# Optimization experiments

Hardware: AMD Instinct MI355X
Metric: run time of the kernel (lower is better)

Reference implementation:

```python
import jax, jax.numpy as jnp
import numpy as np

B, S = 2, 2048
D, H, L = 768, 12, 2
DH = D // H
WIN = 128            # one-sided sliding window
C = WIN              # query chunk size
NC = S // C
FF = 4 * D
V = 50265
SEP_ID = 2
NSEP = 16
G = NSEP + 1         # CLS + all SEP tokens are global
NCLS = 7
HID = 100
NEG = -1e9
SEP_POS = np.arange(1, NSEP + 1) * 120   # fixed [SEP] layout, same every row


def setup_inputs() -> dict:
    key = jax.random.key(0)
    ks = iter(jax.random.split(key, 32))
    def p(shape, scale=0.02):
        return scale * jax.random.normal(next(ks), shape, jnp.float32)
    input_ids = jax.random.randint(next(ks), (B, S), 10, V)
    input_ids = input_ids.at[:, SEP_POS].set(SEP_ID)
    attention_mask = jnp.ones((B, S), jnp.int32)
    return dict(
        input_ids=input_ids, attention_mask=attention_mask,
        tok_emb=p((V, D)), pos_emb=p((S, D)),
        ln_e_g=jnp.ones((D,)), ln_e_b=jnp.zeros((D,)),
        Wq=p((L, D, D)), bq=jnp.zeros((L, D)),
        Wk=p((L, D, D)), bk=jnp.zeros((L, D)),
        Wv=p((L, D, D)), bv=jnp.zeros((L, D)),
        Wo=p((L, D, D)), bo=jnp.zeros((L, D)),
        ln1_g=jnp.ones((L, D)), ln1_b=jnp.zeros((L, D)),
        W1=p((L, D, FF)), b1=jnp.zeros((L, FF)),
        W2=p((L, FF, D)), b2=jnp.zeros((L, D)),
        ln2_g=jnp.ones((L, D)), ln2_b=jnp.zeros((L, D)),
        Wh=p((2 * D, HID)), bh=jnp.zeros((HID,)),
        Wout=p((HID, NCLS)), bout=jnp.zeros((NCLS,)),
    )


def _ln(x, g, b):
    mu = jnp.mean(x, -1, keepdims=True)
    var = jnp.var(x, -1, keepdims=True)
    return (x - mu) * jax.lax.rsqrt(var + 1e-5) * g + b


def forward(input_ids, attention_mask, tok_emb, pos_emb, ln_e_g, ln_e_b,
            Wq, bq, Wk, bk, Wv, bv, Wo, bo, ln1_g, ln1_b,
            W1, b1, W2, b2, ln2_g, ln2_b, Wh, bh, Wout, bout):
    # global positions: CLS + every [SEP] (same layout in every row)
    sep_pos = jnp.nonzero(input_ids[0] == SEP_ID, size=NSEP)[0]          # [NSEP]
    glob = jnp.concatenate([jnp.zeros((1,), sep_pos.dtype), sep_pos])    # [G]

    amask = attention_mask.astype(jnp.float32)                           # [B,S]
    is_glob = jnp.zeros((S,), bool).at[glob].set(True)

    # banded (sliding-window) gather pattern, padded-coordinate indices
    idx = jnp.arange(NC)[:, None] * C + jnp.arange(3 * C)[None, :]       # [NC,3C]
    pos_k = idx - C                                                      # abs key pos
    pos_q = jnp.arange(NC)[:, None] * C + jnp.arange(C)[None, :]         # [NC,C]
    pos_k_c = jnp.clip(pos_k, 0, S - 1)
    band = jnp.abs(pos_k[:, None, :] - pos_q[:, :, None]) <= WIN         # [NC,C,3C]
    inb = (pos_k >= 0) & (pos_k < S)                                     # [NC,3C]
    # global keys are handled by the dedicated global columns -> drop from band
    band = band & (inb & ~is_glob[pos_k_c])[:, None, :]
    km = amask[:, pos_k_c] * inb                                         # [B,NC,3C]
    valid = band[None] & (km[:, :, None, :] > 0)                         # [B,NC,C,3C]
    gmask = amask[:, glob] > 0                                           # [B,G]

    x = tok_emb[input_ids] + pos_emb[None]                               # [B,S,D]
    x = _ln(x, ln_e_g, ln_e_b)

    for l in range(L):
        q = (x @ Wq[l] + bq[l]).reshape(B, S, H, DH).transpose(0, 2, 1, 3) * (DH ** -0.5)
        k = (x @ Wk[l] + bk[l]).reshape(B, S, H, DH).transpose(0, 2, 1, 3)
        v = (x @ Wv[l] + bv[l]).reshape(B, S, H, DH).transpose(0, 2, 1, 3)
        kp = jnp.pad(k, ((0, 0), (0, 0), (C, C), (0, 0)))
        vp = jnp.pad(v, ((0, 0), (0, 0), (C, C), (0, 0)))
        k3 = kp[:, :, idx]                                               # [B,H,NC,3C,DH]
        v3 = vp[:, :, idx]
        qc = q.reshape(B, H, NC, C, DH)
        s_loc = jnp.einsum('bhncd,bhnkd->bhnck', qc, k3)                 # banded scores
        s_loc = jnp.where(valid[:, None], s_loc, NEG)
        kg, vg = k[:, :, glob], v[:, :, glob]                            # [B,H,G,DH]
        s_g = jnp.einsum('bhncd,bhgd->bhncg', qc, kg)
        s_g = jnp.where(gmask[:, None, None, None, :], s_g, NEG)
        p = jax.nn.softmax(jnp.concatenate([s_loc, s_g], axis=-1), axis=-1)
        out = (jnp.einsum('bhnck,bhnkd->bhncd', p[..., :3 * C], v3)
               + jnp.einsum('bhncg,bhgd->bhncd', p[..., 3 * C:], vg))
        out = out.reshape(B, H, S, DH)
        # global query rows attend to the full sequence
        qg = q[:, :, glob]
        s_full = jnp.einsum('bhgd,bhsd->bhgs', qg, k)
        s_full = jnp.where(amask[:, None, None, :] > 0, s_full, NEG)
        out_g = jnp.einsum('bhgs,bhsd->bhgd', jax.nn.softmax(s_full, -1), v)
        out = out.at[:, :, glob, :].set(out_g)
        a = out.transpose(0, 2, 1, 3).reshape(B, S, D) @ Wo[l] + bo[l]
        x = _ln(x + a, ln1_g[l], ln1_b[l])
        h = jax.nn.gelu(x @ W1[l] + b1[l])
        x = _ln(x + h @ W2[l] + b2[l], ln2_g[l], ln2_b[l])

    # core-sentence embeddings: hstack(CLS, interior SEP embeddings)
    core = sep_pos[1:-1]                                                 # [NSEP-2]
    cls = x[:, 0, :]                                                     # [B,D]
    seps = x[:, core, :]                                                 # [B,NSEP-2,D]
    emb = jnp.concatenate([jnp.broadcast_to(cls[:, None], seps.shape), seps], -1)
    emb = emb.reshape(B * (NSEP - 2), 2 * D)
    return jax.nn.relu(emb @ Wh + bh) @ Wout + bout                      # [28, NCLS]


def reference(input_ids, attention_mask, tok_emb, pos_emb, ln_e_g, ln_e_b,
              Wq, bq, Wk, bk, Wv, bv, Wo, bo, ln1_g, ln1_b,
              W1, b1, W2, b2, ln2_g, ln2_b, Wh, bh, Wout, bout):
    return forward(input_ids, attention_mask, tok_emb, pos_emb, ln_e_g, ln_e_b,
                   Wq, bq, Wk, bk, Wv, bv, Wo, bo, ln1_g, ln1_b,
                   W1, b1, W2, b2, ln2_g, ln2_b, Wh, bh, Wout, bout)
```

## Files before the change

kernel.cpp:

```cpp
#include <hip/hip_runtime.h>
#include <hip/hip_bf16.h>
#include <math.h>

#define Sdim 2048
#define Bdim 2
#define Ddim 768
#define Hdim 12
#define DHdim 64
#define Ldim 2
#define Cdim 128
#define NCdim 16
#define FFdim 3072
#define Gdim 17
#define NSEPd 16
#define HIDd 100
#define NCLSd 7
#define SEPID 2
#define MROWS (Bdim*Sdim)
#define QKVS 2304
#define MNSZ (MROWS*Ddim)

typedef __bf16 bf16_t;
typedef bf16_t bf16x8 __attribute__((ext_vector_type(8)));
typedef float f32x4 __attribute__((ext_vector_type(4)));
typedef ushort ushort8v __attribute__((ext_vector_type(8)));

__device__ __forceinline__ ushort f2bf(float f) {
    union { float f; unsigned u; } a; a.f = f;
    unsigned u = a.u;
    unsigned r = (u + 0x7fffu + ((u >> 16) & 1u)) >> 16;
    return (ushort)r;
}
__device__ __forceinline__ float bf2f(ushort h) {
    union { unsigned u; float f; } a; a.u = ((unsigned)h) << 16;
    return a.f;
}
__device__ __forceinline__ void gload16(const ushort* g, ushort* l) {
    __builtin_amdgcn_global_load_lds(
        (const __attribute__((address_space(1))) void*)g,
        (__attribute__((address_space(3))) void*)l, 16, 0, 0);
}

__global__ __launch_bounds__(1024) void k_findsep(const int* __restrict__ ids,
        int* __restrict__ glob, int* __restrict__ isg,
        const float* __restrict__ bq, const float* __restrict__ bk,
        const float* __restrict__ bv, float* __restrict__ bqkv) {
    __shared__ unsigned long long mw[32];
    __shared__ int pfx[32];
    int t = threadIdx.x;
    int flg[2];
    #pragma unroll
    for (int pass = 0; pass < 2; ++pass) {
        int p = pass * 1024 + t;
        int f = (ids[p] == SEPID);
        flg[pass] = f;
        unsigned long long m = __ballot(f);
        if ((t & 63) == 0) mw[pass * 16 + (t >> 6)] = m;
    }
    __syncthreads();
    if (t == 0) {
        int c = 0;
        #pragma unroll
        for (int i = 0; i < 32; ++i) { pfx[i] = c; c += __popcll(mw[i]); }
        glob[0] = 0;
    }
    __syncthreads();
    #pragma unroll
    for (int pass = 0; pass < 2; ++pass) {
        int p = pass * 1024 + t;
        int w = pass * 16 + (t >> 6);
        int lane = t & 63;
        int rank = pfx[w] + __popcll(mw[w] & ((1ull << lane) - 1ull));
        int ig = 0;
        if (flg[pass] && rank < NSEPd) { glob[rank + 1] = p; ig = 1; }
        if (p == 0) ig = 1;
        isg[p] = ig;
    }
    for (int idx = t; idx < Ldim * QKVS; idx += 1024) {
        int l = idx / QKVS, i = idx % QKVS;
        float v = (i < Ddim) ? bq[l * Ddim + i]
                : (i < 2 * Ddim) ? bk[l * Ddim + i - Ddim]
                : bv[l * Ddim + i - 2 * Ddim];
        bqkv[idx] = v;
    }
}

__global__ __launch_bounds__(256) void k_w2bt_all(
        const float* __restrict__ Wq, const float* __restrict__ Wk,
        const float* __restrict__ Wv, const float* __restrict__ Wo,
        const float* __restrict__ W1, const float* __restrict__ W2,
        ushort* __restrict__ wts) {
    const size_t WSMALL = (size_t)Ddim * Ddim;
    const size_t WBIG   = (size_t)Ddim * FFdim;
    const size_t WL     = 4 * WSMALL + 2 * WBIG;
    int bid = blockIdx.x;
    int l = bid / 1728, r = bid % 1728;
    const float* src; ushort* dst; int K, N, tile;
    ushort* base = wts + (size_t)l * WL;
    if (r < 576) {
        int w = r / 144; tile = r % 144; K = Ddim; N = Ddim;
        src = (w == 0 ? Wq : w == 1 ? Wk : w == 2 ? Wv : Wo) + (size_t)l * WSMALL;
        dst = base + (size_t)w * WSMALL;
    } else if (r < 1152) {
        tile = r - 576; K = Ddim; N = FFdim;
        src = W1 + (size_t)l * WBIG; dst = base + 4 * WSMALL;
    } else {
        tile = r - 1152; K = FFdim; N = Ddim;
        src = W2 + (size_t)l * WBIG; dst = base + 4 * WSMALL + WBIG;
    }
    int ntn = N / 64;
    int bn = (tile % ntn) * 64, bk = (tile / ntn) * 64;

    __shared__ float ts[64][65];
    int t = threadIdx.x;
    int rx = t & 63, ry = t >> 6;
    #pragma unroll
    for (int i = 0; i < 16; ++i) {
        int row = ry * 16 + i;
        ts[row][rx] = src[(size_t)(bk + row) * N + bn + rx];
    }
    __syncthreads();
    int wr = t >> 4;
    int k0 = (t & 15) * 4;
    #pragma unroll
    for (int pass = 0; pass < 4; ++pass) {
        int row = pass * 16 + wr;
        ushort4 val;
        val.x = f2bf(ts[k0 + 0][row]);
        val.y = f2bf(ts[k0 + 1][row]);
        val.z = f2bf(ts[k0 + 2][row]);
        val.w = f2bf(ts[k0 + 3][row]);
        *(ushort4*)(&dst[(size_t)(bn + row) * K + bk + k0]) = val;
    }
}

__global__ __launch_bounds__(64) void k_embed(const int* __restrict__ ids,
        const float* __restrict__ tok, const float* __restrict__ pos,
        const float* __restrict__ g, const float* __restrict__ b,
        float* __restrict__ x, ushort* __restrict__ xb) {
    int row = blockIdx.x;
    int s = row & (Sdim - 1);
    long id = ids[row];
    const float4* te = (const float4*)(tok + id * (long)Ddim);
    const float4* pe = (const float4*)(pos + (long)s * Ddim);
    int t = threadIdx.x;
    float4 v[3];
    float ls = 0.f, lq = 0.f;
    #pragma unroll
    for (int i = 0; i < 3; ++i) {
        float4 a = te[i * 64 + t], p = pe[i * 64 + t];
        v[i].x = a.x + p.x; v[i].y = a.y + p.y; v[i].z = a.z + p.z; v[i].w = a.w + p.w;
        ls += v[i].x + v[i].y + v[i].z + v[i].w;
        lq += v[i].x * v[i].x + v[i].y * v[i].y + v[i].z * v[i].z + v[i].w * v[i].w;
    }
    #pragma unroll
    for (int o = 32; o; o >>= 1) { ls += __shfl_xor(ls, o, 64); lq += __shfl_xor(lq, o, 64); }
    float mu = ls / Ddim;
    float var = lq / Ddim - mu * mu;
    float rs = rsqrtf(var + 1e-5f);
    const float4* g4 = (const float4*)g;
    const float4* b4 = (const float4*)b;
    float4* xr = (float4*)(x + (long)row * Ddim);
    ushort4* xbr = (ushort4*)(xb + (long)row * Ddim);
    #pragma unroll
    for (int i = 0; i < 3; ++i) {
        float4 gg = g4[i * 64 + t], bb = b4[i * 64 + t];
        float4 o;
        o.x = (v[i].x - mu) * rs * gg.x + bb.x;
        o.y = (v[i].y - mu) * rs * gg.y + bb.y;
        o.z = (v[i].z - mu) * rs * gg.z + bb.z;
        o.w = (v[i].w - mu) * rs * gg.w + bb.w;
        xr[i * 64 + t] = o;
        ushort4 ob; ob.x = f2bf(o.x); ob.y = f2bf(o.y); ob.z = f2bf(o.z); ob.w = f2bf(o.w);
        xbr[i * 64 + t] = ob;
    }
}

__global__ __launch_bounds__(64) void k_ln_res4(float* __restrict__ x,
        const float* __restrict__ pr4, const float* __restrict__ bias,
        const float* __restrict__ g, const float* __restrict__ b,
        ushort* __restrict__ xb) {
    long row = blockIdx.x;
    int t = threadIdx.x;
    const float4* xr = (const float4*)(x + row * Ddim);
    const float4* p0 = (const float4*)(pr4 + row * Ddim);
    const float4* p1 = (const float4*)(pr4 + (size_t)MNSZ + row * Ddim);
    const float4* p2 = (const float4*)(pr4 + 2 * (size_t)MNSZ + row * Ddim);
    const float4* p3 = (const float4*)(pr4 + 3 * (size_t)MNSZ + row * Ddim);
    const float4* bi = (const float4*)bias;
    float4 v[3];
    float ls = 0.f, lq = 0.f;
    #pragma unroll
    for (int i = 0; i < 3; ++i) {
        int ii = i * 64 + t;
        float4 xa = xr[ii], a0 = p0[ii], a1 = p1[ii], a2 = p2[ii], a3 = p3[ii], bb = bi[ii];
        v[i].x = xa.x + ((a0.x + a1.x) + (a2.x + a3.x)) + bb.x;
        v[i].y = xa.y + ((a0.y + a1.y) + (a2.y + a3.y)) + bb.y;
        v[i].z = xa.z + ((a0.z + a1.z) + (a2.z + a3.z)) + bb.z;
        v[i].w = xa.w + ((a0.w + a1.w) + (a2.w + a3.w)) + bb.w;
        ls += v[i].x + v[i].y + v[i].z + v[i].w;
        lq += v[i].x * v[i].x + v[i].y * v[i].y + v[i].z * v[i].z + v[i].w * v[i].w;
    }
    #pragma unroll
    for (int o = 32; o; o >>= 1) { ls += __shfl_xor(ls, o, 64); lq += __shfl_xor(lq, o, 64); }
    float mu = ls / Ddim;
    float var = lq / Ddim - mu * mu;
    float rs = rsqrtf(var + 1e-5f);
    const float4* g4 = (const float4*)g;
    const float4* b4 = (const float4*)b;
    float4* xw = (float4*)(x + row * Ddim);
    ushort4* xbr = (ushort4*)(xb + row * Ddim);
    #pragma unroll
    for (int i = 0; i < 3; ++i) {
        float4 gg = g4[i * 64 + t], bb = b4[i * 64 + t];
        float4 o;
        o.x = (v[i].x - mu) * rs * gg.x + bb.x;
        o.y = (v[i].y - mu) * rs * gg.y + bb.y;
        o.z = (v[i].z - mu) * rs * gg.z + bb.z;
        o.w = (v[i].w - mu) * rs * gg.w + bb.w;
        xw[i * 64 + t] = o;
        ushort4 ob; ob.x = f2bf(o.x); ob.y = f2bf(o.y); ob.z = f2bf(o.z); ob.w = f2bf(o.w);
        xbr[i * 64 + t] = ob;
    }
}

template<int ACT, int OUTBF16>
__global__ __launch_bounds__(256) void k_gemm_bf16(
        const ushort* __restrict__ A, const ushort* __restrict__ Wt,
        const float* __restrict__ bias, void* __restrict__ Cout,
        int M, int N, int K)
{
    __shared__ ushort As[2][128 * 32];
    __shared__ ushort Bs[2][128 * 32];
    const int t = threadIdx.x;
    const int nwg = gridDim.x * gridDim.y;
    const int wgid = blockIdx.y * gridDim.x + blockIdx.x;
    const int q8 = nwg >> 3, r8 = nwg & 7;
    const int xcd = wgid & 7, idx = wgid >> 3;
    const int swz = (xcd < r8 ? xcd * (q8 + 1) : r8 * (q8 + 1) + (xcd - r8) * q8) + idx;
    const int bm = (swz / gridDim.x) * 128;
    const int bn = (swz % gridDim.x) * 128;
    const int lane = t & 63;
    const int wv = t >> 6;
    const int wm = (wv >> 1) * 64;
    const int wn = (wv & 1) * 64;

    const int srow = t >> 2;
    const int scol = (t & 3) * 8;
    const ushort* gA0 = A + (size_t)(bm + srow) * K + scol;
    const ushort* gA1 = A + (size_t)(bm + 64 + srow) * K + scol;
    const ushort* gB0 = Wt + (size_t)(bn + srow) * K + scol;
    const ushort* gB1 = Wt + (size_t)(bn + 64 + srow) * K + scol;

    f32x4 acc[4][4] = {};
    const int frow = lane & 15;
    const int koff = (lane >> 4) * 8;

    auto stage = [&](int d, int k0) {
        gload16(gA0 + k0, &As[d][t * 8]);
        gload16(gA1 + k0, &As[d][2048 + t * 8]);
        gload16(gB0 + k0, &Bs[d][t * 8]);
        gload16(gB1 + k0, &Bs[d][2048 + t * 8]);
    };

    stage(0, 0);
    __syncthreads();
    const int niter = K / 32;
    int cur = 0;
    for (int it = 0; it < niter; ++it) {
        if (it + 1 < niter) stage(cur ^ 1, (it + 1) * 32);
        bf16x8 af[4], bfv[4];
        #pragma unroll
        for (int mi = 0; mi < 4; ++mi)
            af[mi] = *reinterpret_cast<const bf16x8*>(&As[cur][(wm + mi * 16 + frow) * 32 + koff]);
        #pragma unroll
        for (int ni = 0; ni < 4; ++ni)
            bfv[ni] = *reinterpret_cast<const bf16x8*>(&Bs[cur][(wn + ni * 16 + frow) * 32 + koff]);
        #pragma unroll
        for (int mi = 0; mi < 4; ++mi)
            #pragma unroll
            for (int ni = 0; ni < 4; ++ni)
                acc[mi][ni] = __builtin_amdgcn_mfma_f32_16x16x32_bf16(af[mi], bfv[ni], acc[mi][ni], 0, 0, 0);
        __syncthreads();
        cur ^= 1;
    }
    const int crow0 = (lane >> 4) * 4;
    const int ccol = lane & 15;
    #pragma unroll
    for (int mi = 0; mi < 4; ++mi) {
        #pragma unroll
        for (int ni = 0; ni < 4; ++ni) {
            int gc = bn + wn + ni * 16 + ccol;
            float bv = bias[gc];
            #pragma unroll
            for (int j = 0; j < 4; ++j) {
                int gr = bm + wm + mi * 16 + crow0 + j;
                float v = acc[mi][ni][j] + bv;
                if (ACT == 1) {
                    float y = 0.7978845608f * (v + 0.044715f * v * v * v);
                    float e = __expf(2.f * y);
                    v = v * (1.f - 1.f / (e + 1.f));
                }
                if (OUTBF16) ((ushort*)Cout)[(size_t)gr * N + gc] = f2bf(v);
                else         ((float*)Cout)[(size_t)gr * N + gc] = v;
            }
        }
    }
}

__global__ __launch_bounds__(256) void k_gemm_splitk(
        const ushort* __restrict__ A, const ushort* __restrict__ Wt,
        float* __restrict__ Cpart, int M, int N, int K, int Kper)
{
    __shared__ ushort As[2][128 * 32];
    __shared__ ushort Bs[2][128 * 32];
    const int t = threadIdx.x;
    const int ks = blockIdx.z;
    const int nwg = gridDim.x * gridDim.y;
    const int wgid = blockIdx.y * gridDim.x + blockIdx.x;
    const int q8 = nwg >> 3, r8 = nwg & 7;
    const int xcd = wgid & 7, idx = wgid >> 3;
    const int swz = (xcd < r8 ? xcd * (q8 + 1) : r8 * (q8 + 1) + (xcd - r8) * q8) + idx;
    const int bm = (swz / gridDim.x) * 128;
    const int bn = (swz % gridDim.x) * 128;
    const int lane = t & 63;
    const int wv = t >> 6;
    const int wm = (wv >> 1) * 64;
    const int wn = (wv & 1) * 64;

    const int srow = t >> 2;
    const int scol = (t & 3) * 8;
    const int kbase = ks * Kper;
    const ushort* gA0 = A + (size_t)(bm + srow) * K + kbase + scol;
    const ushort* gA1 = A + (size_t)(bm + 64 + srow) * K + kbase + scol;
    const ushort* gB0 = Wt + (size_t)(bn + srow) * K + kbase + scol;
    const ushort* gB1 = Wt + (size_t)(bn + 64 + srow) * K + kbase + scol;

    f32x4 acc[4][4] = {};
    const int frow = lane & 15;
    const int koff = (lane >> 4) * 8;

    auto stage = [&](int d, int k0) {
        gload16(gA0 + k0, &As[d][t * 8]);
        gload16(gA1 + k0, &As[d][2048 + t * 8]);
        gload16(gB0 + k0, &Bs[d][t * 8]);
        gload16(gB1 + k0, &Bs[d][2048 + t * 8]);
    };

    stage(0, 0);
    __syncthreads();
    const int niter = Kper / 32;
    int cur = 0;
    for (int it = 0; it < niter; ++it) {
        if (it + 1 < niter) stage(cur ^ 1, (it + 1) * 32);
        bf16x8 af[4], bfv[4];
        #pragma unroll
        for (int mi = 0; mi < 4; ++mi)
            af[mi] = *reinterpret_cast<const bf16x8*>(&As[cur][(wm + mi * 16 + frow) * 32 + koff]);
        #pragma unroll
        for (int ni = 0; ni < 4; ++ni)
            bfv[ni] = *reinterpret_cast<const bf16x8*>(&Bs[cur][(wn + ni * 16 + frow) * 32 + koff]);
        #pragma unroll
        for (int mi = 0; mi < 4; ++mi)
            #pragma unroll
            for (int ni = 0; ni < 4; ++ni)
                acc[mi][ni] = __builtin_amdgcn_mfma_f32_16x16x32_bf16(af[mi], bfv[ni], acc[mi][ni], 0, 0, 0);
        __syncthreads();
        cur ^= 1;
    }
    float* outp = Cpart + (size_t)ks * M * N;
    const int crow0 = (lane >> 4) * 4;
    const int ccol = lane & 15;
    #pragma unroll
    for (int mi = 0; mi < 4; ++mi) {
        #pragma unroll
        for (int ni = 0; ni < 4; ++ni) {
            int gc = bn + wn + ni * 16 + ccol;
            #pragma unroll
            for (int j = 0; j < 4; ++j) {
                int gr = bm + wm + mi * 16 + crow0 + j;
                outp[(size_t)gr * N + gc] = acc[mi][ni][j];
            }
        }
    }
}

__global__ __launch_bounds__(256) void k_attn_mfma(
        const ushort* __restrict__ qkv, const int* __restrict__ isg,
        const int* __restrict__ glob, const int* __restrict__ amask,
        ushort* __restrict__ ao)
{
    const int n = blockIdx.x, h = blockIdx.y, b = blockIdx.z;
    const int t = threadIdx.x;
    const int lane = t & 63, wv = t >> 6;
    const int R0 = b * Sdim;
    const int l15 = lane & 15, l4 = lane >> 4;

    __shared__ ushort Kb[64 * 64];
    __shared__ ushort Vt[64 * 72];
    __shared__ ushort Plds[4][32 * 72];
    __shared__ float  maskLDS[448];

    for (int i = t; i < 448; i += 256) {
        int ok;
        if (i < 384) {
            int pos = n * Cdim + i - Cdim;
            ok = (pos >= 0 && pos < Sdim);
            if (ok) ok = (amask[b * Sdim + pos] != 0) && (isg[pos] == 0);
        } else {
            int g = i - 384;
            int gp = (g < Gdim) ? glob[g] : 0;
            ok = (g < Gdim) && (amask[b * Sdim + gp] != 0);
        }
        maskLDS[i] = ok ? 0.f : -1e9f;
    }

    bf16x8 qf[2][2];
    #pragma unroll
    for (int qi = 0; qi < 2; ++qi)
        #pragma unroll
        for (int kh = 0; kh < 2; ++kh)
            qf[qi][kh] = *reinterpret_cast<const bf16x8*>(
                qkv + (size_t)(R0 + n * Cdim + wv * 32 + qi * 16 + l15) * QKVS
                    + h * DHdim + kh * 32 + l4 * 8);

    f32x4 accO[2][4] = {};
    float mrow[2][4], lrow[2][4];
    #pragma unroll
    for (int qi = 0; qi < 2; ++qi)
        #pragma unroll
        for (int j = 0; j < 4; ++j) { mrow[qi][j] = -1e30f; lrow[qi][j] = 0.f; }

    const int jj = t >> 3;
    const int c16 = t & 7;

    auto ldone = [&](int j, ushort8v& kr, ushort8v& vr) {
        int pos = 0; bool ok;
        if (j < 384) { pos = n * Cdim + j - Cdim; ok = (pos >= 0 && pos < Sdim); }
        else { int g = j - 384; ok = (g < Gdim); if (ok) pos = glob[g]; }
        ushort8v z = {};
        if (ok) {
            const ushort* kp = qkv + (size_t)(R0 + pos) * QKVS + Ddim + h * DHdim + c16 * 8;
            kr = *reinterpret_cast<const ushort8v*>(kp);
            vr = *reinterpret_cast<const ushort8v*>(kp + Ddim);
        } else { kr = z; vr = z; }
    };

    ushort8v kr0, kr1, vr0, vr1, nk0 = {}, nk1 = {}, nv0 = {}, nv1 = {};
    ldone(jj, kr0, vr0);
    ldone(jj + 32, kr1, vr1);

    for (int kt = 0; kt < 7; ++kt) {
        __syncthreads();
        *reinterpret_cast<ushort8v*>(&Kb[jj * 64 + ((c16 ^ (jj & 7)) * 8)]) = kr0;
        *reinterpret_cast<ushort8v*>(&Kb[(jj + 32) * 64 + ((c16 ^ (jj & 7)) * 8)]) = kr1;
        #pragma unroll
        for (int e = 0; e < 8; ++e) {
            Vt[(c16 * 8 + e) * 72 + jj] = vr0[e];
            Vt[(c16 * 8 + e) * 72 + 32 + jj] = vr1[e];
        }
        if (kt < 6) {
            int base_j = (kt + 1) * 64 + jj;
            ldone(base_j, nk0, nv0);
            ldone(base_j + 32, nk1, nv1);
        }
        __syncthreads();

        bool active = (kt == 6) || ((kt * 64 + 63 >= wv * 32) && (kt * 64 <= wv * 32 + 287));
        if (active) {
            bf16x8 kf[4][2];
            #pragma unroll
            for (int kj = 0; kj < 4; ++kj) {
                int key = kj * 16 + l15;
                #pragma unroll
                for (int kh = 0; kh < 2; ++kh) {
                    int cc = (kh * 4 + l4) ^ (key & 7);
                    kf[kj][kh] = *reinterpret_cast<const bf16x8*>(&Kb[key * 64 + cc * 8]);
                }
            }
            float ma[4];
            #pragma unroll
            for (int kj = 0; kj < 4; ++kj) ma[kj] = maskLDS[kt * 64 + kj * 16 + l15];

            #pragma unroll
            for (int qi = 0; qi < 2; ++qi) {
                f32x4 s[4] = {};
                #pragma unroll
                for (int kj = 0; kj < 4; ++kj)
                    #pragma unroll
                    for (int kh = 0; kh < 2; ++kh)
                        s[kj] = __builtin_amdgcn_mfma_f32_16x16x32_bf16(qf[qi][kh], kf[kj][kh], s[kj], 0, 0, 0);

                float sf[4][4];
                #pragma unroll
                for (int kj = 0; kj < 4; ++kj) {
                    int key = kt * 64 + kj * 16 + l15;
                    #pragma unroll
                    for (int j = 0; j < 4; ++j) {
                        int cq = wv * 32 + qi * 16 + l4 * 4 + j;
                        float sv = s[kj][j] * 0.125f + ma[kj];
                        bool band = (key >= 384) || ((unsigned)(key - cq) <= 256u);
                        sf[kj][j] = band ? sv : sv - 1e9f;
                    }
                }
                float mnew[4], corr[4];
                #pragma unroll
                for (int j = 0; j < 4; ++j) {
                    float v = fmaxf(fmaxf(sf[0][j], sf[1][j]), fmaxf(sf[2][j], sf[3][j]));
                    v = fmaxf(v, __shfl_xor(v, 1, 64));
                    v = fmaxf(v, __shfl_xor(v, 2, 64));
                    v = fmaxf(v, __shfl_xor(v, 4, 64));
                    v = fmaxf(v, __shfl_xor(v, 8, 64));
                    mnew[j] = fmaxf(mrow[qi][j], v);
                    corr[j] = __expf(mrow[qi][j] - mnew[j]);
                    mrow[qi][j] = mnew[j];
                }
                float ps[4][4];
                #pragma unroll
                for (int kj = 0; kj < 4; ++kj)
                    #pragma unroll
                    for (int j = 0; j < 4; ++j)
                        ps[kj][j] = __expf(sf[kj][j] - mnew[j]);
                #pragma unroll
                for (int j = 0; j < 4; ++j) {
                    float r = (ps[0][j] + ps[1][j]) + (ps[2][j] + ps[3][j]);
                    r += __shfl_xor(r, 1, 64);
                    r += __shfl_xor(r, 2, 64);
                    r += __shfl_xor(r, 4, 64);
                    r += __shfl_xor(r, 8, 64);
                    lrow[qi][j] = lrow[qi][j] * corr[j] + r;
                }
                bool need = (corr[0] < 1.f) || (corr[1] < 1.f) || (corr[2] < 1.f) || (corr[3] < 1.f);
                if (__any((int)need)) {
                    #pragma unroll
                    for (int dt = 0; dt < 4; ++dt)
                        #pragma unroll
                        for (int j = 0; j < 4; ++j)
                            accO[qi][dt][j] *= corr[j];
                }
                #pragma unroll
                for (int kj = 0; kj < 4; ++kj)
                    #pragma unroll
                    for (int j = 0; j < 4; ++j)
                        Plds[wv][(qi * 16 + l4 * 4 + j) * 72 + kj * 16 + l15] = f2bf(ps[kj][j]);
            }
            #pragma unroll
            for (int qi = 0; qi < 2; ++qi) {
                #pragma unroll
                for (int ks = 0; ks < 2; ++ks) {
                    bf16x8 af = *reinterpret_cast<const bf16x8*>(
                        &Plds[wv][(qi * 16 + l15) * 72 + ks * 32 + l4 * 8]);
                    #pragma unroll
                    for (int dt = 0; dt < 4; ++dt) {
                        bf16x8 vf = *reinterpret_cast<const bf16x8*>(
                            &Vt[(dt * 16 + l15) * 72 + ks * 32 + l4 * 8]);
                        accO[qi][dt] = __builtin_amdgcn_mfma_f32_16x16x32_bf16(af, vf, accO[qi][dt], 0, 0, 0);
                    }
                }
            }
        }
        kr0 = nk0; kr1 = nk1; vr0 = nv0; vr1 = nv1;
    }

    #pragma unroll
    for (int qi = 0; qi < 2; ++qi) {
        float inv[4];
        #pragma unroll
        for (int j = 0; j < 4; ++j) inv[j] = 1.f / lrow[qi][j];
        #pragma unroll
        for (int dt = 0; dt < 4; ++dt) {
            #pragma unroll
            for (int j = 0; j < 4; ++j) {
                int crow = n * Cdim + wv * 32 + qi * 16 + l4 * 4 + j;
                ao[(size_t)(R0 + crow) * Ddim + h * DHdim + dt * 16 + l15] =
                    f2bf(accO[qi][dt][j] * inv[j]);
            }
        }
    }
}

__global__ __launch_bounds__(256) void k_attn_glob(const ushort* __restrict__ qkv,
        const int* __restrict__ glob, const int* __restrict__ amask,
        ushort* __restrict__ ao) {
    int g = blockIdx.x, h = blockIdx.y, b = blockIdx.z;
    __shared__ float sc[Sdim];
    __shared__ float qs[DHdim];
    __shared__ float redm[4], reds[4];
    __shared__ float part[32][DHdim];
    int t = threadIdx.x;
    int qr = glob[g];
    const int R0 = b * Sdim;
    if (t < DHdim)
        qs[t] = bf2f(qkv[(size_t)(R0 + qr) * QKVS + h * DHdim + t]) * 0.125f;
    __syncthreads();
    float lm = -1e30f;
    for (int s0 = t; s0 < Sdim; s0 += 256) {
        const ushort8v* kr = (const ushort8v*)(qkv + (size_t)(R0 + s0) * QKVS + Ddim + h * DHdim);
        float s = 0.f;
        #pragma unroll
        for (int cc = 0; cc < 8; ++cc) {
            ushort8v kv = kr[cc];
            #pragma unroll
            for (int e = 0; e < 8; ++e) s += qs[cc * 8 + e] * bf2f(kv[e]);
        }
        if (amask[b * Sdim + s0] == 0) s = -1e30f;
        sc[s0] = s;
        lm = fmaxf(lm, s);
    }
    #pragma unroll
    for (int o = 32; o; o >>= 1) lm = fmaxf(lm, __shfl_xor(lm, o, 64));
    if ((t & 63) == 0) redm[t >> 6] = lm;
    __syncthreads();
    float mx = fmaxf(fmaxf(redm[0], redm[1]), fmaxf(redm[2], redm[3]));
    float lsum = 0.f;
    for (int s0 = t; s0 < Sdim; s0 += 256) {
        float p = __expf(sc[s0] - mx);
        sc[s0] = p; lsum += p;
    }
    #pragma unroll
    for (int o = 32; o; o >>= 1) lsum += __shfl_xor(lsum, o, 64);
    if ((t & 63) == 0) reds[t >> 6] = lsum;
    __syncthreads();
    float l = reds[0] + reds[1] + reds[2] + reds[3];
    int chunk = t >> 3, dg = t & 7;
    float a[8] = {};
    for (int r = chunk * 64; r < chunk * 64 + 64; ++r) {
        float p = sc[r];
        ushort8v vv = *(const ushort8v*)(qkv + (size_t)(R0 + r) * QKVS + 2 * Ddim + h * DHdim + dg * 8);
        #pragma unroll
        for (int e = 0; e < 8; ++e) a[e] += p * bf2f(vv[e]);
    }
    #pragma unroll
    for (int e = 0; e < 8; ++e) part[chunk][dg * 8 + e] = a[e];
    __syncthreads();
    if (t < DHdim) {
        float o = 0.f;
        #pragma unroll
        for (int c = 0; c < 32; ++c) o += part[c][t];
        ao[(size_t)(R0 + qr) * Ddim + h * DHdim + t] = f2bf(o / l);
    }
}

__global__ __launch_bounds__(256) void k_head(const float* __restrict__ x,
        const int* __restrict__ glob, const float* __restrict__ Wh,
        const float* __restrict__ bh, const float* __restrict__ Wout,
        const float* __restrict__ bout, float* __restrict__ out) {
    int i = blockIdx.x;
    int b = i / 14, j = i % 14;
    __shared__ float emb[2 * Ddim];
    __shared__ float hp[2][128];
    __shared__ float hid[HIDd];
    int t = threadIdx.x;
    int p = glob[j + 2];
    for (int d = t; d < Ddim; d += 256) {
        emb[d] = x[(long)b * Sdim * Ddim + d];
        emb[Ddim + d] = x[((long)b * Sdim + p) * Ddim + d];
    }
    __syncthreads();
    int nn = t & 127, half = t >> 7;
    float s = 0.f;
    if (nn < HIDd) {
        int k0 = half * Ddim;
        for (int k1 = 0; k1 < Ddim; ++k1) s += emb[k0 + k1] * Wh[(k0 + k1) * HIDd + nn];
    }
    hp[half][nn] = s;
    __syncthreads();
    if (t < HIDd) hid[t] = fmaxf(hp[0][t] + hp[1][t] + bh[t], 0.f);
    __syncthreads();
    if (t < NCLSd) {
        float s2 = bout[t];
        for (int o = 0; o < HIDd; ++o) s2 += hid[o] * Wout[o * NCLSd + t];
        out[i * NCLSd + t] = s2;
    }
}

extern "C" void kernel_launch(void* const* d_in, const int* in_sizes, int n_in,
                              void* d_out, int out_size, void* d_ws, size_t ws_size,
                              hipStream_t stream) {
    const int*   ids   = (const int*)d_in[0];
    const int*   am    = (const int*)d_in[1];
    const float* tok   = (const float*)d_in[2];
    const float* pos   = (const float*)d_in[3];
    const float* lneg  = (const float*)d_in[4];
    const float* lneb  = (const float*)d_in[5];
    const float* Wq    = (const float*)d_in[6];
    const float* bq    = (const float*)d_in[7];
    const float* Wk    = (const float*)d_in[8];
    const float* bk    = (const float*)d_in[9];
    const float* Wv    = (const float*)d_in[10];
    const float* bv    = (const float*)d_in[11];
    const float* Wo    = (const float*)d_in[12];
    const float* bo    = (const float*)d_in[13];
    const float* ln1g  = (const float*)d_in[14];
    const float* ln1b  = (const float*)d_in[15];
    const float* W1    = (const float*)d_in[16];
    const float* b1    = (const float*)d_in[17];
    const float* W2    = (const float*)d_in[18];
    const float* b2    = (const float*)d_in[19];
    const float* ln2g  = (const float*)d_in[20];
    const float* ln2b  = (const float*)d_in[21];
    const float* Wh    = (const float*)d_in[22];
    const float* bh    = (const float*)d_in[23];
    const float* Wout  = (const float*)d_in[24];
    const float* bout  = (const float*)d_in[25];
    float* out = (float*)d_out;

    char* ws = (char*)d_ws;
    const size_t SZ = (size_t)MROWS * Ddim * sizeof(float);
    const size_t HB = SZ / 2;
    size_t off = 0;
    float*  x    = (float*)(ws + off);  off += SZ;
    float*  pr4  = (float*)(ws + off);  off += 4 * SZ;
    ushort* xb   = (ushort*)(ws + off); off += HB;
    ushort* qkvB = (ushort*)(ws + off); off += (size_t)MROWS * QKVS * 2;
    ushort* aoB  = (ushort*)(ws + off); off += HB;
    ushort* hh   = (ushort*)(ws + off); off += (size_t)MROWS * FFdim * 2;
    const size_t WSMALL = (size_t)Ddim * Ddim;
    const size_t WBIG   = (size_t)Ddim * FFdim;
    const size_t WL     = 4 * WSMALL + 2 * WBIG;
    ushort* wts = (ushort*)(ws + off); off += WL * Ldim * 2;
    float* bqkv = (float*)(ws + off);  off += Ldim * QKVS * sizeof(float);
    int* glob = (int*)(ws + off); off += 256;
    int* isg  = (int*)(ws + off);

    k_findsep<<<1, 1024, 0, stream>>>(ids, glob, isg, bq, bk, bv, bqkv);
    k_w2bt_all<<<3456, 256, 0, stream>>>(Wq, Wk, Wv, Wo, W1, W2, wts);
    k_embed<<<MROWS, 64, 0, stream>>>(ids, tok, pos, lneg, lneb, x, xb);

    dim3 gQKV(QKVS / 128, MROWS / 128);
    dim3 gFF(FFdim / 128, MROWS / 128);
    dim3 gSK(Ddim / 128, MROWS / 128, 4);
    dim3 gloc(NCdim, Hdim, Bdim);
    dim3 gglb(Gdim, Hdim, Bdim);

    for (int l = 0; l < Ldim; ++l) {
        ushort* base = wts + l * WL;
        ushort* Wqkvt = base;
        ushort* Wot = base + 3 * WSMALL;
        ushort* W1t = base + 4 * WSMALL;
        ushort* W2t = base + 4 * WSMALL + WBIG;
        k_gemm_bf16<0,1><<<gQKV, 256, 0, stream>>>(xb, Wqkvt, bqkv + l * QKVS, qkvB, MROWS, QKVS, Ddim);
        k_attn_mfma<<<gloc, 256, 0, stream>>>(qkvB, isg, glob, am, aoB);
        k_attn_glob<<<gglb, 256, 0, stream>>>(qkvB, glob, am, aoB);
        k_gemm_splitk<<<gSK, 256, 0, stream>>>(aoB, Wot, pr4, MROWS, Ddim, Ddim, Ddim / 4);
        k_ln_res4<<<MROWS, 64, 0, stream>>>(x, pr4, bo + l * Ddim, ln1g + l * Ddim, ln1b + l * Ddim, xb);
        k_gemm_bf16<1,1><<<gFF, 256, 0, stream>>>(xb, W1t, b1 + l * FFdim, hh, MROWS, FFdim, Ddim);
        k_gemm_splitk<<<gSK, 256, 0, stream>>>(hh, W2t, pr4, MROWS, Ddim, FFdim, FFdim / 4);
        k_ln_res4<<<MROWS, 64, 0, stream>>>(x, pr4, b2 + l * Ddim, ln2g + l * Ddim, ln2b + l * Ddim, xb);
    }
    k_head<<<Bdim * (NSEPd - 2), 256, 0, stream>>>(x, glob, Wh, bh, Wout, bout, out);
}
```

Before: 473.5 us.

## Fuse local and global attention into one launch with split-sequence global partials

Local sliding-window attention blocks and global-token attention blocks now run in a single kernel launch, with global attention split across 8 sequence chunks per (batch, head). Each chunk computes all 17 global queries at once and writes partial max/sum/accumulator values, which a small reduction kernel combines. Local blocks skip writing rows that belong to global tokens to avoid a write race. The aim is more parallelism for the global path (previously 17x12x2 blocks each scanning the full sequence) and overlap with local work, at the cost of an extra launch, a workspace buffer and uncoalesced strided V reads in the partial kernel.

```diff
diff --git a/kernel.cpp b/kernel.cpp
--- a/kernel.cpp
+++ b/kernel.cpp
@@ -19,6 +19,8 @@
 #define MROWS (Bdim*Sdim)
 #define QKVS 2304
 #define MNSZ (MROWS*Ddim)
+#define NLOC (NCdim*Hdim*Bdim)
+#define NGP  (8*Hdim*Bdim)
 
 typedef __bf16 bf16_t;
 typedef bf16_t bf16x8 __attribute__((ext_vector_type(8)));
@@ -385,260 +387,293 @@
     }
 }
 
-__global__ __launch_bounds__(256) void k_attn_mfma(
+__global__ __launch_bounds__(256) void k_attn_fused(
         const ushort* __restrict__ qkv, const int* __restrict__ isg,
         const int* __restrict__ glob, const int* __restrict__ amask,
-        ushort* __restrict__ ao)
+        ushort* __restrict__ ao, float* __restrict__ gpart)
 {
-    const int n = blockIdx.x, h = blockIdx.y, b = blockIdx.z;
+    __shared__ __align__(16) char smem[38400];
+    const int bid = blockIdx.x;
     const int t = threadIdx.x;
-    const int lane = t & 63, wv = t >> 6;
-    const int R0 = b * Sdim;
-    const int l15 = lane & 15, l4 = lane >> 4;
-
-    __shared__ ushort Kb[64 * 64];
-    __shared__ ushort Vt[64 * 72];
-    __shared__ ushort Plds[4][32 * 72];
-    __shared__ float  maskLDS[448];
-
-    for (int i = t; i < 448; i += 256) {
-        int ok;
-        if (i < 384) {
-            int pos = n * Cdim + i - Cdim;
-            ok = (pos >= 0 && pos < Sdim);
-            if (ok) ok = (amask[b * Sdim + pos] != 0) && (isg[pos] == 0);
-        } else {
-            int g = i - 384;
-            int gp = (g < Gdim) ? glob[g] : 0;
-            ok = (g < Gdim) && (amask[b * Sdim + gp] != 0);
-        }
-        maskLDS[i] = ok ? 0.f : -1e9f;
-    }
-
-    bf16x8 qf[2][2];
-    #pragma unroll
-    for (int qi = 0; qi < 2; ++qi)
-        #pragma unroll
-        for (int kh = 0; kh < 2; ++kh)
-            qf[qi][kh] = *reinterpret_cast<const bf16x8*>(
-                qkv + (size_t)(R0 + n * Cdim + wv * 32 + qi * 16 + l15) * QKVS
-                    + h * DHdim + kh * 32 + l4 * 8);
-
-    f32x4 accO[2][4] = {};
-    float mrow[2][4], lrow[2][4];
-    #pragma unroll
-    for (int qi = 0; qi < 2; ++qi)
-        #pragma unroll
-        for (int j = 0; j < 4; ++j) { mrow[qi][j] = -1e30f; lrow[qi][j] = 0.f; }
-
-    const int jj = t >> 3;
-    const int c16 = t & 7;
-
-    auto ldone = [&](int j, ushort8v& kr, ushort8v& vr) {
-        int pos = 0; bool ok;
-        if (j < 384) { pos = n * Cdim + j - Cdim; ok = (pos >= 0 && pos < Sdim); }
-        else { int g = j - 384; ok = (g < Gdim); if (ok) pos = glob[g]; }
-        ushort8v z = {};
-        if (ok) {
-            const ushort* kp = qkv + (size_t)(R0 + pos) * QKVS + Ddim + h * DHdim + c16 * 8;
-            kr = *reinterpret_cast<const ushort8v*>(kp);
-            vr = *reinterpret_cast<const ushort8v*>(kp + Ddim);
-        } else { kr = z; vr = z; }
-    };
-
-    ushort8v kr0, kr1, vr0, vr1, nk0 = {}, nk1 = {}, nv0 = {}, nv1 = {};
-    ldone(jj, kr0, vr0);
-    ldone(jj + 32, kr1, vr1);
-
-    for (int kt = 0; kt < 7; ++kt) {
-        __syncthreads();
-        *reinterpret_cast<ushort8v*>(&Kb[jj * 64 + ((c16 ^ (jj & 7)) * 8)]) = kr0;
-        *reinterpret_cast<ushort8v*>(&Kb[(jj + 32) * 64 + ((c16 ^ (jj & 7)) * 8)]) = kr1;
-        #pragma unroll
-        for (int e = 0; e < 8; ++e) {
-            Vt[(c16 * 8 + e) * 72 + jj] = vr0[e];
-            Vt[(c16 * 8 + e) * 72 + 32 + jj] = vr1[e];
-        }
-        if (kt < 6) {
-            int base_j = (kt + 1) * 64 + jj;
-            ldone(base_j, nk0, nv0);
-            ldone(base_j + 32, nk1, nv1);
-        }
-        __syncthreads();
-
-        bool active = (kt == 6) || ((kt * 64 + 63 >= wv * 32) && (kt * 64 <= wv * 32 + 287));
-        if (active) {
-            bf16x8 kf[4][2];
-            #pragma unroll
-            for (int kj = 0; kj < 4; ++kj) {
-                int key = kj * 16 + l15;
-                #pragma unroll
-                for (int kh = 0; kh < 2; ++kh) {
-                    int cc = (kh * 4 + l4) ^ (key & 7);
-                    kf[kj][kh] = *reinterpret_cast<const bf16x8*>(&Kb[key * 64 + cc * 8]);
-                }
+
+    if (bid < NLOC) {
+        ushort* Kb   = (ushort*)smem;
+        ushort* Vt   = (ushort*)(smem + 8192);
+        ushort* Plds = (ushort*)(smem + 17408);
+        float* maskLDS = (float*)(smem + 35840);
+        int*   rowg    = (int*)(smem + 37632);
+
+        const int n = bid & 15, h = (bid >> 4) % Hdim, b = bid / (16 * Hdim);
+        const int lane = t & 63, wv = t >> 6;
+        const int R0 = b * Sdim;
+        const int l15 = lane & 15, l4 = lane >> 4;
+
+        for (int i = t; i < 448; i += 256) {
+            int ok;
+            if (i < 384) {
+                int pos = n * Cdim + i - Cdim;
+                ok = (pos >= 0 && pos < Sdim);
+                if (ok) ok = (amask[b * Sdim + pos] != 0) && (isg[pos] == 0);
+            } else {
+                int g = i - 384;
+                int gp = (g < Gdim) ? glob[g] : 0;
+                ok = (g < Gdim) && (amask[b * Sdim + gp] != 0);
             }
-            float ma[4];
-            #pragma unroll
-            for (int kj = 0; kj < 4; ++kj) ma[kj] = maskLDS[kt * 64 + kj * 16 + l15];
-
-            #pragma unroll
-            for (int qi = 0; qi < 2; ++qi) {
-                f32x4 s[4] = {};
-                #pragma unroll
-                for (int kj = 0; kj < 4; ++kj)
-                    #pragma unroll
-                    for (int kh = 0; kh < 2; ++kh)
-                        s[kj] = __builtin_amdgcn_mfma_f32_16x16x32_bf16(qf[qi][kh], kf[kj][kh], s[kj], 0, 0, 0);
-
-                float sf[4][4];
+            maskLDS[i] = ok ? 0.f : -1e9f;
+        }
+        if (t < 128) rowg[t] = isg[n * Cdim + t];
+
+        bf16x8 qf[2][2];
+        #pragma unroll
+        for (int qi = 0; qi < 2; ++qi)
+            #pragma unroll
+            for (int kh = 0; kh < 2; ++kh)
+                qf[qi][kh] = *reinterpret_cast<const bf16x8*>(
+                    qkv + (size_t)(R0 + n * Cdim + wv * 32 + qi * 16 + l15) * QKVS
+                        + h * DHdim + kh * 32 + l4 * 8);
+
+        f32x4 accO[2][4] = {};
+        float mrow[2][4], lrow[2][4];
+        #pragma unroll
+        for (int qi = 0; qi < 2; ++qi)
+            #pragma unroll
+            for (int j = 0; j < 4; ++j) { mrow[qi][j] = -1e30f; lrow[qi][j] = 0.f; }
+
+        const int jj = t >> 3;
+        const int c16 = t & 7;
+
+        auto ldone = [&](int j, ushort8v& kr, ushort8v& vr) {
+            int pos = 0; bool ok;
+            if (j < 384) { pos = n * Cdim + j - Cdim; ok = (pos >= 0 && pos < Sdim); }
+            else { int g = j - 384; ok = (g < Gdim); if (ok) pos = glob[g]; }
+            ushort8v z = {};
+            if (ok) {
+                const ushort* kp = qkv + (size_t)(R0 + pos) * QKVS + Ddim + h * DHdim + c16 * 8;
+                kr = *reinterpret_cast<const ushort8v*>(kp);
+                vr = *reinterpret_cast<const ushort8v*>(kp + Ddim);
+            } else { kr = z; vr = z; }
+        };
+
+        ushort8v kr0, kr1, vr0, vr1, nk0 = {}, nk1 = {}, nv0 = {}, nv1 = {};
+        ldone(jj, kr0, vr0);
+        ldone(jj + 32, kr1, vr1);
+
+        for (int kt = 0; kt < 7; ++kt) {
+            __syncthreads();
+            *reinterpret_cast<ushort8v*>(&Kb[jj * 64 + ((c16 ^ (jj & 7)) * 8)]) = kr0;
+            *reinterpret_cast<ushort8v*>(&Kb[(jj + 32) * 64 + ((c16 ^ (jj & 7)) * 8)]) = kr1;
+            #pragma unroll
+            for (int e = 0; e < 8; ++e) {
+                Vt[(c16 * 8 + e) * 72 + jj] = vr0[e];
+                Vt[(c16 * 8 + e) * 72 + 32 + jj] = vr1[e];
+            }
+            if (kt < 6) {
+                int base_j = (kt + 1) * 64 + jj;
+                ldone(base_j, nk0, nv0);
+                ldone(base_j + 32, nk1, nv1);
+            }
+            __syncthreads();
+
+            bool active = (kt == 6) || ((kt * 64 + 63 >= wv * 32) && (kt * 64 <= wv * 32 + 287));
+            if (active) {
+                bf16x8 kf[4][2];
                 #pragma unroll
                 for (int kj = 0; kj < 4; ++kj) {
-                    int key = kt * 64 + kj * 16 + l15;
-                    #pragma unroll
-                    for (int j = 0; j < 4; ++j) {
-                        int cq = wv * 32 + qi * 16 + l4 * 4 + j;
-                        float sv = s[kj][j] * 0.125f + ma[kj];
-                        bool band = (key >= 384) || ((unsigned)(key - cq) <= 256u);
-                        sf[kj][j] = band ? sv : sv - 1e9f;
+                    int key = kj * 16 + l15;
+                    #pragma unroll
+                    for (int kh = 0; kh < 2; ++kh) {
+                        int cc = (kh * 4 + l4) ^ (key & 7);
+                        kf[kj][kh] = *reinterpret_cast<const bf16x8*>(&Kb[key * 64 + cc * 8]);
                     }
                 }
-                float mnew[4], corr[4];
+                float ma[4];
                 #pragma unroll
-                for (int j = 0; j < 4; ++j) {
-                    float v = fmaxf(fmaxf(sf[0][j], sf[1][j]), fmaxf(sf[2][j], sf[3][j]));
-                    v = fmaxf(v, __shfl_xor(v, 1, 64));
-                    v = fmaxf(v, __shfl_xor(v, 2, 64));
-                    v = fmaxf(v, __shfl_xor(v, 4, 64));
-                    v = fmaxf(v, __shfl_xor(v, 8, 64));
-                    mnew[j] = fmaxf(mrow[qi][j], v);
-                    corr[j] = __expf(mrow[qi][j] - mnew[j]);
-                    mrow[qi][j] = mnew[j];
-                }
-                float ps[4][4];
+                for (int kj = 0; kj < 4; ++kj) ma[kj] = maskLDS[kt * 64 + kj * 16 + l15];
+
                 #pragma unroll
-                for (int kj = 0; kj < 4; ++kj)
-                    #pragma unroll
-                    for (int j = 0; j < 4; ++j)
-                        ps[kj][j] = __expf(sf[kj][j] - mnew[j]);
-                #pragma unroll
-                for (int j = 0; j < 4; ++j) {
-                    float r = (ps[0][j] + ps[1][j]) + (ps[2][j] + ps[3][j]);
-                    r += __shfl_xor(r, 1, 64);
-                    r += __shfl_xor(r, 2, 64);
-                    r += __shfl_xor(r, 4, 64);
-                    r += __shfl_xor(r, 8, 64);
-                    lrow[qi][j] = lrow[qi][j] * corr[j] + r;
-                }
-                bool need = (corr[0] < 1.f) || (corr[1] < 1.f) || (corr[2] < 1.f) || (corr[3] < 1.f);
-                if (__any((int)need)) {
-                    #pragma unroll
-                    for (int dt = 0; dt < 4; ++dt)
+                for (int qi = 0; qi < 2; ++qi) {
+                    f32x4 s[4] = {};
+                    #pragma unroll
+                    for (int kj = 0; kj < 4; ++kj)
+                        #pragma unroll
+                        for (int kh = 0; kh < 2; ++kh)
+                            s[kj] = __builtin_amdgcn_mfma_f32_16x16x32_bf16(qf[qi][kh], kf[kj][kh], s[kj], 0, 0, 0);
+
+                    float sf[4][4];
+                    #pragma unroll
+                    for (int kj = 0; kj < 4; ++kj) {
+                        int key = kt * 64 + kj * 16 + l15;
+                        #pragma unroll
+                        for (int j = 0; j < 4; ++j) {
+                            int cq = wv * 32 + qi * 16 + l4 * 4 + j;
+                            float sv = s[kj][j] * 0.125f + ma[kj];
+                            bool band = (key >= 384) || ((unsigned)(key - cq) <= 256u);
+                            sf[kj][j] = band ? sv : sv - 1e9f;
+                        }
+                    }
+                    float mnew[4], corr[4];
+                    #pragma unroll
+                    for (int j = 0; j < 4; ++j) {
+                        float v = fmaxf(fmaxf(sf[0][j], sf[1][j]), fmaxf(sf[2][j], sf[3][j]));
+                        v = fmaxf(v, __shfl_xor(v, 1, 64));
+                        v = fmaxf(v, __shfl_xor(v, 2, 64));
+                        v = fmaxf(v, __shfl_xor(v, 4, 64));
+                        v = fmaxf(v, __shfl_xor(v, 8, 64));
+                        mnew[j] = fmaxf(mrow[qi][j], v);
+                        corr[j] = __expf(mrow[qi][j] - mnew[j]);
+                        mrow[qi][j] = mnew[j];
+                    }
+                    float ps[4][4];
+                    #pragma unroll
+                    for (int kj = 0; kj < 4; ++kj)
                         #pragma unroll
                         for (int j = 0; j < 4; ++j)
-                            accO[qi][dt][j] *= corr[j];
+                            ps[kj][j] = __expf(sf[kj][j] - mnew[j]);
+                    #pragma unroll
+                    for (int j = 0; j < 4; ++j) {
+                        float r = (ps[0][j] + ps[1][j]) + (ps[2][j] + ps[3][j]);
+                        r += __shfl_xor(r, 1, 64);
+                        r += __shfl_xor(r, 2, 64);
+                        r += __shfl_xor(r, 4, 64);
+                        r += __shfl_xor(r, 8, 64);
+                        lrow[qi][j] = lrow[qi][j] * corr[j] + r;
+                    }
+                    bool need = (corr[0] < 1.f) || (corr[1] < 1.f) || (corr[2] < 1.f) || (corr[3] < 1.f);
+                    if (__any((int)need)) {
+                        #pragma unroll
+                        for (int dt = 0; dt < 4; ++dt)
+                            #pragma unroll
+                            for (int j = 0; j < 4; ++j)
+                                accO[qi][dt][j] *= corr[j];
+                    }
+                    #pragma unroll
+                    for (int kj = 0; kj < 4; ++kj)
+                        #pragma unroll
+                        for (int j = 0; j < 4; ++j)
+                            Plds[wv * 2304 + (qi * 16 + l4 * 4 + j) * 72 + kj * 16 + l15] = f2bf(ps[kj][j]);
                 }
                 #pragma unroll
-                for (int kj = 0; kj < 4; ++kj)
-                    #pragma unroll
-                    for (int j = 0; j < 4; ++j)
-                        Plds[wv][(qi * 16 + l4 * 4 + j) * 72 + kj * 16 + l15] = f2bf(ps[kj][j]);
-            }
-            #pragma unroll
-            for (int qi = 0; qi < 2; ++qi) {
-                #pragma unroll
-                for (int ks = 0; ks < 2; ++ks) {
-                    bf16x8 af = *reinterpret_cast<const bf16x8*>(
-                        &Plds[wv][(qi * 16 + l15) * 72 + ks * 32 + l4 * 8]);
-                    #pragma unroll
-                    for (int dt = 0; dt < 4; ++dt) {
-                        bf16x8 vf = *reinterpret_cast<const bf16x8*>(
-                            &Vt[(dt * 16 + l15) * 72 + ks * 32 + l4 * 8]);
-                        accO[qi][dt] = __builtin_amdgcn_mfma_f32_16x16x32_bf16(af, vf, accO[qi][dt], 0, 0, 0);
+                for (int qi = 0; qi < 2; ++qi) {
+                    #pragma unroll
+                    for (int ks = 0; ks < 2; ++ks) {
+                        bf16x8 af = *reinterpret_cast<const bf16x8*>(
+                            &Plds[wv * 2304 + (qi * 16 + l15) * 72 + ks * 32 + l4 * 8]);
+                        #pragma unroll
+                        for (int dt = 0; dt < 4; ++dt) {
+                            bf16x8 vf = *reinterpret_cast<const bf16x8*>(
+                                &Vt[(dt * 16 + l15) * 72 + ks * 32 + l4 * 8]);
+                            accO[qi][dt] = __builtin_amdgcn_mfma_f32_16x16x32_bf16(af, vf, accO[qi][dt], 0, 0, 0);
+                        }
                     }
                 }
             }
-        }
-        kr0 = nk0; kr1 = nk1; vr0 = nv0; vr1 = nv1;
-    }
-
-    #pragma unroll
-    for (int qi = 0; qi < 2; ++qi) {
-        float inv[4];
-        #pragma unroll
-        for (int j = 0; j < 4; ++j) inv[j] = 1.f / lrow[qi][j];
-        #pragma unroll
-        for (int dt = 0; dt < 4; ++dt) {
-            #pragma unroll
-            for (int j = 0; j < 4; ++j) {
-                int crow = n * Cdim + wv * 32 + qi * 16 + l4 * 4 + j;
-                ao[(size_t)(R0 + crow) * Ddim + h * DHdim + dt * 16 + l15] =
-                    f2bf(accO[qi][dt][j] * inv[j]);
+            kr0 = nk0; kr1 = nk1; vr0 = nv0; vr1 = nv1;
+        }
+
+        #pragma unroll
+        for (int qi = 0; qi < 2; ++qi) {
+            float inv[4];
+            #pragma unroll
+            for (int j = 0; j < 4; ++j) inv[j] = 1.f / lrow[qi][j];
+            #pragma unroll
+            for (int dt = 0; dt < 4; ++dt) {
+                #pragma unroll
+                for (int j = 0; j < 4; ++j) {
+                    int lr = wv * 32 + qi * 16 + l4 * 4 + j;
+                    if (!rowg[lr]) {
+                        ao[(size_t)(R0 + n * Cdim + lr) * Ddim + h * DHdim + dt * 16 + l15] =
+                            f2bf(accO[qi][dt][j] * inv[j]);
+                    }
+                }
             }
         }
-    }
-}
-
-__global__ __launch_bounds__(256) void k_attn_glob(const ushort* __restrict__ qkv,
-        const int* __restrict__ glob, const int* __restrict__ amask,
-        ushort* __restrict__ ao) {
+    } else {
+        float* qsg = (float*)smem;
+        float* sP  = (float*)(smem + 4352);
+        float* mg  = (float*)(smem + 21760);
+        float* lg  = mg + 17;
+
+        const int e = bid - NLOC;
+        const int sc = e & 7, h = (e >> 3) % Hdim, b = e / (8 * Hdim);
+        const int R0 = b * Sdim;
+
+        for (int i = t; i < Gdim * DHdim; i += 256) {
+            int g = i >> 6, d = i & 63;
+            qsg[i] = bf2f(qkv[(size_t)(R0 + glob[g]) * QKVS + h * DHdim + d]) * 0.125f;
+        }
+        __syncthreads();
+
+        const int r = sc * 256 + t;
+        float s[Gdim] = {};
+        {
+            const ushort8v* kr = (const ushort8v*)(qkv + (size_t)(R0 + r) * QKVS + Ddim + h * DHdim);
+            #pragma unroll
+            for (int cc = 0; cc < 8; ++cc) {
+                ushort8v kv = kr[cc];
+                #pragma unroll
+                for (int ee = 0; ee < 8; ++ee) {
+                    float kf = bf2f(kv[ee]);
+                    int d = cc * 8 + ee;
+                    #pragma unroll
+                    for (int g = 0; g < Gdim; ++g) s[g] += qsg[g * 64 + d] * kf;
+                }
+            }
+        }
+        bool okr = (amask[b * Sdim + r] != 0);
+        #pragma unroll
+        for (int g = 0; g < Gdim; ++g) sP[g * 256 + t] = okr ? s[g] : -1e9f;
+        __syncthreads();
+
+        const int wvv = t >> 6, lane = t & 63;
+        for (int g = wvv; g < Gdim; g += 4) {
+            float a0 = sP[g * 256 + lane];
+            float a1 = sP[g * 256 + 64 + lane];
+            float a2 = sP[g * 256 + 128 + lane];
+            float a3 = sP[g * 256 + 192 + lane];
+            float mx = fmaxf(fmaxf(a0, a1), fmaxf(a2, a3));
+            #pragma unroll
+            for (int o = 32; o; o >>= 1) mx = fmaxf(mx, __shfl_xor(mx, o, 64));
+            float e0 = __expf(a0 - mx), e1 = __expf(a1 - mx);
+            float e2 = __expf(a2 - mx), e3 = __expf(a3 - mx);
+            float es = (e0 + e1) + (e2 + e3);
+            #pragma unroll
+            for (int o = 32; o; o >>= 1) es += __shfl_xor(es, o, 64);
+            sP[g * 256 + lane] = e0;
+            sP[g * 256 + 64 + lane] = e1;
+            sP[g * 256 + 128 + lane] = e2;
+            sP[g * 256 + 192 + lane] = e3;
+            if (lane == 0) { mg[g] = mx; lg[g] = es; }
+        }
+        __syncthreads();
+
+        float* pr = gpart + (((size_t)b * Hdim + h) * 8 + sc) * (Gdim * 66);
+        for (int o = t; o < Gdim * DHdim; o += 256) {
+            int g = o >> 6, d = o & 63;
+            const ushort* vp = qkv + (size_t)(R0 + sc * 256) * QKVS + 2 * Ddim + h * DHdim + d;
+            float acc = 0.f;
+            for (int k = 0; k < 256; ++k)
+                acc += sP[g * 256 + k] * bf2f(vp[(size_t)k * QKVS]);
+            pr[g * 66 + 2 + d] = acc;
+        }
+        if (t < Gdim) { pr[t * 66 + 0] = mg[t]; pr[t * 66 + 1] = lg[t]; }
+    }
+}
+
+__global__ __launch_bounds__(64) void k_globred(const float* __restrict__ gpart,
+        const int* __restrict__ glob, ushort* __restrict__ ao) {
     int g = blockIdx.x, h = blockIdx.y, b = blockIdx.z;
-    __shared__ float sc[Sdim];
-    __shared__ float qs[DHdim];
-    __shared__ float redm[4], reds[4];
-    __shared__ float part[32][DHdim];
-    int t = threadIdx.x;
-    int qr = glob[g];
-    const int R0 = b * Sdim;
-    if (t < DHdim)
-        qs[t] = bf2f(qkv[(size_t)(R0 + qr) * QKVS + h * DHdim + t]) * 0.125f;
-    __syncthreads();
-    float lm = -1e30f;
-    for (int s0 = t; s0 < Sdim; s0 += 256) {
-        const ushort8v* kr = (const ushort8v*)(qkv + (size_t)(R0 + s0) * QKVS + Ddim + h * DHdim);
-        float s = 0.f;
-        #pragma unroll
-        for (int cc = 0; cc < 8; ++cc) {
-            ushort8v kv = kr[cc];
-            #pragma unroll
-            for (int e = 0; e < 8; ++e) s += qs[cc * 8 + e] * bf2f(kv[e]);
-        }
-        if (amask[b * Sdim + s0] == 0) s = -1e30f;
-        sc[s0] = s;
-        lm = fmaxf(lm, s);
-    }
-    #pragma unroll
-    for (int o = 32; o; o >>= 1) lm = fmaxf(lm, __shfl_xor(lm, o, 64));
-    if ((t & 63) == 0) redm[t >> 6] = lm;
-    __syncthreads();
-    float mx = fmaxf(fmaxf(redm[0], redm[1]), fmaxf(redm[2], redm[3]));
-    float lsum = 0.f;
-    for (int s0 = t; s0 < Sdim; s0 += 256) {
-        float p = __expf(sc[s0] - mx);
-        sc[s0] = p; lsum += p;
-    }
-    #pragma unroll
-    for (int o = 32; o; o >>= 1) lsum += __shfl_xor(lsum, o, 64);
-    if ((t & 63) == 0) reds[t >> 6] = lsum;
-    __syncthreads();
-    float l = reds[0] + reds[1] + reds[2] + reds[3];
-    int chunk = t >> 3, dg = t & 7;
-    float a[8] = {};
-    for (int r = chunk * 64; r < chunk * 64 + 64; ++r) {
-        float p = sc[r];
-        ushort8v vv = *(const ushort8v*)(qkv + (size_t)(R0 + r) * QKVS + 2 * Ddim + h * DHdim + dg * 8);
-        #pragma unroll
-        for (int e = 0; e < 8; ++e) a[e] += p * bf2f(vv[e]);
-    }
-    #pragma unroll
-    for (int e = 0; e < 8; ++e) part[chunk][dg * 8 + e] = a[e];
-    __syncthreads();
-    if (t < DHdim) {
-        float o = 0.f;
-        #pragma unroll
-        for (int c = 0; c < 32; ++c) o += part[c][t];
-        ao[(size_t)(R0 + qr) * Ddim + h * DHdim + t] = f2bf(o / l);
-    }
+    int lane = threadIdx.x;
+    float M = -1e30f, L = 0.f, A = 0.f;
+    for (int sc = 0; sc < 8; ++sc) {
+        const float* pp = gpart + (((size_t)b * Hdim + h) * 8 + sc) * (Gdim * 66) + g * 66;
+        float m = pp[0], l = pp[1], a = pp[2 + lane];
+        float nM = fmaxf(M, m);
+        float c1 = __expf(M - nM), c2 = __expf(m - nM);
+        L = L * c1 + l * c2;
+        A = A * c1 + a * c2;
+        M = nM;
+    }
+    ao[(size_t)(b * Sdim + glob[g]) * Ddim + h * DHdim + lane] = f2bf(A / L);
 }
 
 __global__ __launch_bounds__(256) void k_head(const float* __restrict__ x,
@@ -720,6 +755,7 @@
     const size_t WL     = 4 * WSMALL + 2 * WBIG;
     ushort* wts = (ushort*)(ws + off); off += WL * Ldim * 2;
     float* bqkv = (float*)(ws + off);  off += Ldim * QKVS * sizeof(float);
+    float* gpart = (float*)(ws + off); off += (size_t)Bdim * Hdim * 8 * Gdim * 66 * sizeof(float);
     int* glob = (int*)(ws + off); off += 256;
     int* isg  = (int*)(ws + off);
 
@@ -730,8 +766,7 @@
     dim3 gQKV(QKVS / 128, MROWS / 128);
     dim3 gFF(FFdim / 128, MROWS / 128);
     dim3 gSK(Ddim / 128, MROWS / 128, 4);
-    dim3 gloc(NCdim, Hdim, Bdim);
-    dim3 gglb(Gdim, Hdim, Bdim);
+    dim3 gred(Gdim, Hdim, Bdim);
 
     for (int l = 0; l < Ldim; ++l) {
         ushort* base = wts + l * WL;
@@ -740,8 +775,8 @@
         ushort* W1t = base + 4 * WSMALL;
         ushort* W2t = base + 4 * WSMALL + WBIG;
         k_gemm_bf16<0,1><<<gQKV, 256, 0, stream>>>(xb, Wqkvt, bqkv + l * QKVS, qkvB, MROWS, QKVS, Ddim);
-        k_attn_mfma<<<gloc, 256, 0, stream>>>(qkvB, isg, glob, am, aoB);
-        k_attn_glob<<<gglb, 256, 0, stream>>>(qkvB, glob, am, aoB);
+        k_attn_fused<<<NLOC + NGP, 256, 0, stream>>>(qkvB, isg, glob, am, aoB, gpart);
+        k_globred<<<gred, 64, 0, stream>>>(gpart, glob, aoB);
         k_gemm_splitk<<<gSK, 256, 0, stream>>>(aoB, Wot, pr4, MROWS, Ddim, Ddim, Ddim / 4);
         k_ln_res4<<<MROWS, 64, 0, stream>>>(x, pr4, bo + l * Ddim, ln1g + l * Ddim, ln1b + l * Ddim, xb);
         k_gemm_bf16<1,1><<<gFF, 256, 0, stream>>>(xb, W1t, b1 + l * FFdim, hh, MROWS, FFdim, Ddim);
```

New measurement: 478.0 us. Within noise of the previous version (+0.9%).
